# Performance work log

Hardware: AMD Instinct MI355X
Metric: run time of the kernel (lower is better)

Reference implementation:

```python
import jax, jax.numpy as jnp
import numpy as np

N, E, IN, H, OUT = 100000, 600000, 128, 128, 64
BN_EPS = 1e-5


def setup_inputs() -> dict:
    key = jax.random.key(0)
    ks = jax.random.split(key, 8)
    def lin(k, i, o):
        return jax.random.normal(k, (i, o), jnp.float32) / np.float32(np.sqrt(i))
    return {
        "x": jax.random.normal(ks[0], (N, IN), jnp.float32),
        "edge_index": jax.random.randint(ks[1], (2, E), 0, N, dtype=jnp.int64),
        "W1": lin(ks[2], IN, H), "b1": jnp.zeros((H,), jnp.float32),
        "gamma": jnp.ones((H,), jnp.float32), "beta": jnp.zeros((H,), jnp.float32),
        "W2": lin(ks[3], H, H), "b2": jnp.zeros((H,), jnp.float32),
        "Wm1": lin(ks[4], H, H), "bm1": jnp.zeros((H,), jnp.float32),
        "Wm2": lin(ks[5], H, OUT), "bm2": jnp.zeros((OUT,), jnp.float32),
    }


def reference(x, edge_index, W1, b1, gamma, beta, W2, b2, Wm1, bm1, Wm2, bm2):
    # GINConv: h = MLP((1 + eps) * x + sum_{j in N(i)} x_j), eps = 0 (train_eps=False)
    src = edge_index[0]
    dst = edge_index[1]  # PyG aggregates messages at edge_index[1]
    agg = jax.ops.segment_sum(x[src], dst, num_segments=x.shape[0])  # [N, IN]
    h = agg + x
    # inner MLP: Linear -> BatchNorm (batch stats) -> ReLU -> Linear
    h = h @ W1 + b1
    mean = jnp.mean(h, axis=0)
    var = jnp.var(h, axis=0)
    h = (h - mean) * jax.lax.rsqrt(var + BN_EPS) * gamma + beta
    h = jax.nn.relu(h)
    h = h @ W2 + b2
    h = jax.nn.relu(h)  # .relu() after conv
    # output MLP (norm=None, dropout=0.5 -> identity at inference): Linear -> ReLU -> Linear
    h = jax.nn.relu(h @ Wm1 + bm1)
    return h @ Wm2 + bm2
```

## Files before the change

kernel.cpp:

```cpp
#include <hip/hip_runtime.h>
#include <hip/hip_bf16.h>
#include <stdint.h>

#define NNODES 100000
#define NEDGES 600000
#define SCAN_CHUNK 1024
#define SCAN_NB 98

typedef __attribute__((ext_vector_type(8))) short bf16x8;
typedef __attribute__((ext_vector_type(4))) float f32x4;
typedef __attribute__((ext_vector_type(4))) unsigned int u32x4;

__device__ inline float b2f(short b) {
    union { unsigned u; float f; } v;
    v.u = ((unsigned)(unsigned short)b) << 16;
    return v.f;
}
__device__ inline short f2b(float f) {
    union { float f; unsigned u; } v;
    v.f = f;
    unsigned r = (v.u + 0x7FFFu + ((v.u >> 16) & 1u)) >> 16;
    return (short)r;
}
__device__ inline unsigned packbf(float lo, float hi) {
    return ((unsigned)(unsigned short)f2b(hi) << 16) | (unsigned)(unsigned short)f2b(lo);
}
__device__ inline void accw(float& a, float& b, unsigned w) {
    union { unsigned u; float f; } x, y;
    x.u = w << 16;
    y.u = w & 0xFFFF0000u;
    a += x.f;
    b += y.f;
}
__device__ inline int swz(int row, int kbyte) {
    return (row * 256 + kbyte) ^ ((row & 7) << 4);
}
#define MFMA16(a, b, c) __builtin_amdgcn_mfma_f32_16x16x32_bf16(a, b, c, 0, 0, 0)

__device__ inline void stage_lds(const short* __restrict__ g, short* s, int w, int l, int n) {
#pragma unroll
    for (int i = 0; i < n; ++i) {
        int base = i * 4096 + w * 1024;
        __builtin_amdgcn_global_load_lds(
            (const __attribute__((address_space(1))) void*)((const char*)g + base + l * 16),
            (__attribute__((address_space(3))) void*)((char*)s + base), 16, 0, 0);
    }
}

__global__ __launch_bounds__(256) void k_prep(const float* __restrict__ x,
                                              const float* __restrict__ W1,
                                              const float* __restrict__ W2,
                                              const float* __restrict__ Wm1,
                                              const float* __restrict__ Wm2,
                                              short* __restrict__ xb, short* __restrict__ Wt,
                                              int* __restrict__ pos, float* __restrict__ stats) {
    int i = blockIdx.x * 256 + threadIdx.x;
    if (i < (NNODES + 1) * 16) {
        bf16x8 o = (bf16x8){0, 0, 0, 0, 0, 0, 0, 0};
        if (i < NNODES * 16) {
            const float4* p = (const float4*)(x + (size_t)i * 8);
            float4 a = p[0], b = p[1];
            o[0] = f2b(a.x); o[1] = f2b(a.y); o[2] = f2b(a.z); o[3] = f2b(a.w);
            o[4] = f2b(b.x); o[5] = f2b(b.y); o[6] = f2b(b.z); o[7] = f2b(b.w);
        }
        *(bf16x8*)(xb + (size_t)i * 8) = o;
    }
    if (i < NNODES) pos[i] = 0;
    if (i < 57344) {
        int jj, lane, kt, ct;
        const float* W;
        int ldw, off;
        if (i < 16384) { off = i; W = W1; ldw = 128; }
        else if (i < 32768) { off = i - 16384; W = W2; ldw = 128; }
        else if (i < 49152) { off = i - 32768; W = Wm1; ldw = 128; }
        else { off = i - 49152; W = Wm2; ldw = 64; }
        jj = off & 7;
        lane = (off >> 3) & 63;
        kt = (off >> 9) & 3;
        ct = (off >> 11) & 7;
        int lr = lane & 15, hi = lane >> 4;
        int c = ct * 16 + lr;
        int k = kt * 32 + hi * 8 + jj;
        Wt[i] = f2b(W[k * ldw + c]);
    }
    if (i < 256) stats[i] = 0.0f;
}


__global__ __launch_bounds__(256) void k_hist(const int* __restrict__ ei, int* __restrict__ cnt) {
    int e = blockIdx.x * 256 + threadIdx.x;
    if (e < NEDGES) atomicAdd(&cnt[ei[NEDGES + e]], 1);
}

__global__ __launch_bounds__(256) void k_scan1(const int* __restrict__ cnt, int* __restrict__ bsums) {
    __shared__ int sd[256];
    int b = blockIdx.x, t = threadIdx.x;
    int base = b * SCAN_CHUNK + t * 4;
    int s = 0;
#pragma unroll
    for (int i = 0; i < 4; ++i) {
        int idx = base + i;
        if (idx < NNODES) s += cnt[idx];
    }
    sd[t] = s;
    __syncthreads();
    for (int off = 128; off > 0; off >>= 1) {
        if (t < off) sd[t] += sd[t + off];
        __syncthreads();
    }
    if (t == 0) bsums[b] = sd[0];
}

__global__ __launch_bounds__(64) void k_scan2(int* __restrict__ bsums, int* __restrict__ rowptr) {
    if (threadIdx.x == 0 && blockIdx.x == 0) {
        int run = 0;
        for (int b = 0; b < SCAN_NB; ++b) {
            int v = bsums[b];
            bsums[b] = run;
            run += v;
        }
        rowptr[NNODES] = run;
    }
}

__global__ __launch_bounds__(256) void k_scan3(const int* __restrict__ cnt,
                                               const int* __restrict__ bsums,
                                               int* __restrict__ rowptr, int* __restrict__ pos) {
    __shared__ int sd[256];
    int b = blockIdx.x, t = threadIdx.x;
    int base = b * SCAN_CHUNK + t * 4;
    int v[4];
    int s = 0;
#pragma unroll
    for (int i = 0; i < 4; ++i) {
        int idx = base + i;
        v[i] = (idx < NNODES) ? cnt[idx] : 0;
        s += v[i];
    }
    sd[t] = s;
    __syncthreads();
    for (int off = 1; off < 256; off <<= 1) {
        int val = (t >= off) ? sd[t - off] : 0;
        __syncthreads();
        sd[t] += val;
        __syncthreads();
    }
    int run = sd[t] - s + bsums[b];
#pragma unroll
    for (int i = 0; i < 4; ++i) {
        int idx = base + i;
        if (idx < NNODES) {
            rowptr[idx] = run;
            pos[idx] = run;
            run += v[i];
        }
    }
}

__global__ __launch_bounds__(256) void k_fill(const int* __restrict__ ei, int* __restrict__ pos,
                                              int* __restrict__ elist) {
    int e = blockIdx.x * 256 + threadIdx.x;
    if (e >= NEDGES) return;
    int src = ei[e];
    int dst = ei[NEDGES + e];
    int p = atomicAdd(&pos[dst], 1);
    elist[p] = src;
}

__global__ __launch_bounds__(512, 8) void k_aggstats(const short* __restrict__ xb,
                                                     const int* __restrict__ rowptr,
                                                     const int* __restrict__ elist,
                                                     const short* __restrict__ W1pk,
                                                     short* __restrict__ bufb,
                                                     float* __restrict__ stats) {
    __shared__ __align__(16) short tile[64 * 128];
    __shared__ float Sred[2][2][128];

    int t = threadIdx.x, w = t >> 6, lane = t & 63;
    int sub = lane & 31, half = lane >> 5;
    int node0 = blockIdx.x * 64;
    int nb = node0 + w * 8;
    const uint2* xr = (const uint2*)xb;

    int vr = rowptr[min(nb + min(lane, 8), NNODES)];
    int beg_all = __shfl(vr, 0);
    int tot_e = __shfl(vr, 8) - beg_all;

    int o_i[8], t_i[8];
#pragma unroll
    for (int i = 0; i < 8; ++i) {
        int beg = __shfl(vr, i);
        int end = __shfl(vr, i + 1);
        o_i[i] = beg - beg_all;
        t_i[i] = end - beg + 1;
    }

    if (tot_e <= 128) {
        int ej0 = (lane < tot_e) ? elist[beg_all + lane] : NNODES;
        int ej1 = (64 + lane < tot_e) ? elist[beg_all + 64 + lane] : NNODES;
#pragma unroll
        for (int i = 0; i < 8; ++i) {
            int n = nb + i;
            int total = t_i[i];
            float a0 = 0.f, a1 = 0.f, a2 = 0.f, a3 = 0.f;
            for (int base = 0; base < total; base += 8) {
                uint2 v[4];
#pragma unroll
                for (int k = 0; k < 4; ++k) {
                    int j = base + 2 * k + half;
                    int p = o_i[i] + j - 1;
                    int s0 = __shfl(ej0, p & 63);
                    int s1 = __shfl(ej1, p & 63);
                    int src = (p < 64) ? s0 : s1;
                    src = (j == 0) ? n : src;
                    src = (j < total && n < NNODES) ? src : NNODES;
                    v[k] = xr[(size_t)src * 32 + sub];
                }
#pragma unroll
                for (int k = 0; k < 4; ++k) {
                    accw(a0, a1, v[k].x);
                    accw(a2, a3, v[k].y);
                }
            }
            a0 += __shfl_xor(a0, 32);
            a1 += __shfl_xor(a1, 32);
            a2 += __shfl_xor(a2, 32);
            a3 += __shfl_xor(a3, 32);
            if (half == 0) {
                int row = w * 8 + i;
                int b8 = sub * 8;
                int off = swz(row, b8 & ~15) + (b8 & 8);
                uint2 o;
                o.x = packbf(a0, a1);
                o.y = packbf(a2, a3);
                *(uint2*)((char*)tile + off) = o;
            }
        }
    } else {
#pragma unroll
        for (int i = 0; i < 8; ++i) {
            int n = nb + i;
            int total = t_i[i];
            int beg = beg_all + o_i[i];
            float a0 = 0.f, a1 = 0.f, a2 = 0.f, a3 = 0.f;
            if (n < NNODES) {
                for (int base = 0; base < total; base += 64) {
                    int j = base + lane;
                    int ej = NNODES;
                    if (j < total) ej = (j == 0) ? n : elist[beg + j - 1];
                    int cnt = min(64, total - base);
                    int pairs = (cnt + 1) >> 1;
                    for (int ii = 0; ii < pairs; ii += 4) {
                        int j0 = 2 * ii + half;
                        int r0 = __shfl(ej, j0);
                        int r1 = __shfl(ej, j0 + 2);
                        int r2 = __shfl(ej, j0 + 4);
                        int r3 = __shfl(ej, j0 + 6);
                        uint2 v0 = xr[(size_t)r0 * 32 + sub];
                        uint2 v1 = xr[(size_t)r1 * 32 + sub];
                        uint2 v2 = xr[(size_t)r2 * 32 + sub];
                        uint2 v3 = xr[(size_t)r3 * 32 + sub];
                        accw(a0, a1, v0.x); accw(a2, a3, v0.y);
                        accw(a0, a1, v1.x); accw(a2, a3, v1.y);
                        accw(a0, a1, v2.x); accw(a2, a3, v2.y);
                        accw(a0, a1, v3.x); accw(a2, a3, v3.y);
                    }
                }
            }
            a0 += __shfl_xor(a0, 32);
            a1 += __shfl_xor(a1, 32);
            a2 += __shfl_xor(a2, 32);
            a3 += __shfl_xor(a3, 32);
            if (half == 0) {
                int row = w * 8 + i;
                int b8 = sub * 8;
                int off = swz(row, b8 & ~15) + (b8 & 8);
                uint2 o;
                o.x = packbf(a0, a1);
                o.y = packbf(a2, a3);
                *(uint2*)((char*)tile + off) = o;
            }
        }
    }
    __syncthreads();

    {
        int row = t >> 3, chunk = t & 7;
        int gr = node0 + row;
        if (gr < NNODES) {
            bf16x8 c0 = *(const bf16x8*)((char*)tile + swz(row, chunk * 32));
            bf16x8 c1 = *(const bf16x8*)((char*)tile + swz(row, chunk * 32 + 16));
            *(bf16x8*)(bufb + (size_t)gr * 128 + chunk * 16) = c0;
            *(bf16x8*)(bufb + (size_t)gr * 128 + chunk * 16 + 8) = c1;
        }
    }

    {
        int lr = lane & 15, hi = lane >> 4;
        int rg = w & 1, cg = w >> 1;
        f32x4 acc[2][2];
#pragma unroll
        for (int r = 0; r < 2; ++r)
#pragma unroll
            for (int c = 0; c < 2; ++c) acc[r][c] = (f32x4){0.f, 0.f, 0.f, 0.f};
#pragma unroll
        for (int kb = 0; kb < 4; ++kb) {
            int kbyte = kb * 64 + hi * 16;
            bf16x8 af[2], bw[2];
#pragma unroll
            for (int r = 0; r < 2; ++r)
                af[r] = *(const bf16x8*)((char*)tile + swz(rg * 32 + r * 16 + lr, kbyte));
#pragma unroll
            for (int c = 0; c < 2; ++c)
                bw[c] = *(const bf16x8*)(W1pk + (((cg * 2 + c) * 4 + kb) * 64 + lane) * 8);
#pragma unroll
            for (int r = 0; r < 2; ++r)
#pragma unroll
                for (int c = 0; c < 2; ++c) acc[r][c] = MFMA16(af[r], bw[c], acc[r][c]);
        }
        float s[2], q[2];
#pragma unroll
        for (int c = 0; c < 2; ++c) { s[c] = 0.f; q[c] = 0.f; }
#pragma unroll
        for (int c = 0; c < 2; ++c)
#pragma unroll
            for (int r = 0; r < 2; ++r)
#pragma unroll
                for (int rr = 0; rr < 4; ++rr) {
                    float v = acc[r][c][rr];
                    s[c] += v;
                    q[c] += v * v;
                }
#pragma unroll
        for (int c = 0; c < 2; ++c) {
            s[c] += __shfl_xor(s[c], 16); s[c] += __shfl_xor(s[c], 32);
            q[c] += __shfl_xor(q[c], 16); q[c] += __shfl_xor(q[c], 32);
        }
        if (lane < 16) {
#pragma unroll
            for (int c = 0; c < 2; ++c) {
                int col = (cg * 2 + c) * 16 + lane;
                Sred[0][rg][col] = s[c];
                Sred[1][rg][col] = q[c];
            }
        }
    }
    __syncthreads();
    if (t < 128) {
        atomicAdd(stats + t, Sred[0][0][t] + Sred[0][1][t]);
        atomicAdd(stats + 128 + t, Sred[1][0][t] + Sred[1][1][t]);
    }
}

__global__ __launch_bounds__(256, 4) void k_mlp(const short* __restrict__ bufb,
                                                const float* __restrict__ stats,
                                                const float* __restrict__ gamma,
                                                const float* __restrict__ beta,
                                                const short* __restrict__ Wt,
                                                const float* __restrict__ b2,
                                                const float* __restrict__ bm1,
                                                const float* __restrict__ bm2,
                                                float* __restrict__ out) {
    __shared__ __align__(16) short wbuf[16384];
    __shared__ float scl[3][128], shf[3][128], bm2s[64];

    int t = threadIdx.x, w = t >> 6, l = t & 63;
    int lr = l & 15, hi = l >> 4;
    size_t node0 = (size_t)blockIdx.x * 128 + w * 32;

    stage_lds(Wt, wbuf, w, l, 8);
    if (t < 128) {
        float mean = stats[t] * (1.0f / NNODES);
        float var = fmaxf(stats[128 + t] * (1.0f / NNODES) - mean * mean, 0.0f);
        float inv = rsqrtf(var + 1e-5f);
        float sc = gamma[t] * inv;
        scl[0][t] = sc;
        shf[0][t] = beta[t] - mean * sc;
        scl[1][t] = 1.0f;
        shf[1][t] = b2[t];
        scl[2][t] = 1.0f;
        shf[2][t] = bm1[t];
    }
    if (t < 64) bm2s[t] = bm2[t];

    bf16x8 bvA[4], bvB[4];
#pragma unroll
    for (int kt = 0; kt < 4; ++kt) {
        bvA[kt] = *(const bf16x8*)(bufb + (node0 + lr) * 128 + kt * 32 + hi * 8);
        bvB[kt] = *(const bf16x8*)(bufb + (node0 + 16 + lr) * 128 + kt * 32 + hi * 8);
    }
    __syncthreads();

    unsigned pwA[8][2], pwB[8][2];

    for (int g = 0; g < 3; ++g) {
#pragma unroll
        for (int ch = 0; ch < 2; ++ch) {
            f32x4 aA[4], aB[4];
#pragma unroll
            for (int cc = 0; cc < 4; ++cc) {
                aA[cc] = (f32x4){0.f, 0.f, 0.f, 0.f};
                aB[cc] = (f32x4){0.f, 0.f, 0.f, 0.f};
            }
#pragma unroll
            for (int kt = 0; kt < 4; ++kt) {
                bf16x8 wv[4];
#pragma unroll
                for (int cc = 0; cc < 4; ++cc)
                    wv[cc] = *(const bf16x8*)(wbuf + ((((ch * 4 + cc) * 4) + kt) * 64 + l) * 8);
#pragma unroll
                for (int cc = 0; cc < 4; ++cc) {
                    aA[cc] = MFMA16(wv[cc], bvA[kt], aA[cc]);
                    aB[cc] = MFMA16(wv[cc], bvB[kt], aB[cc]);
                }
            }
#pragma unroll
            for (int cc = 0; cc < 4; ++cc) {
                int ct = ch * 4 + cc;
                int c0 = ct * 16 + hi * 4;
                float4 s4 = *(const float4*)&scl[g][c0];
                float4 h4 = *(const float4*)&shf[g][c0];
                pwA[ct][0] = packbf(fmaxf(aA[cc][0] * s4.x + h4.x, 0.f),
                                    fmaxf(aA[cc][1] * s4.y + h4.y, 0.f));
                pwA[ct][1] = packbf(fmaxf(aA[cc][2] * s4.z + h4.z, 0.f),
                                    fmaxf(aA[cc][3] * s4.w + h4.w, 0.f));
                pwB[ct][0] = packbf(fmaxf(aB[cc][0] * s4.x + h4.x, 0.f),
                                    fmaxf(aB[cc][1] * s4.y + h4.y, 0.f));
                pwB[ct][1] = packbf(fmaxf(aB[cc][2] * s4.z + h4.z, 0.f),
                                    fmaxf(aB[cc][3] * s4.w + h4.w, 0.f));
            }
        }
        __syncthreads();
        if (g < 2) stage_lds(Wt + (g + 1) * 16384, wbuf, w, l, 8);
        else       stage_lds(Wt + 49152, wbuf, w, l, 4);

        {
            int h2 = hi >> 1, h1 = hi & 1;
#pragma unroll
            for (int kt = 0; kt < 4; ++kt) {
                unsigned nwA[4], nwB[4];
#pragma unroll
                for (int jp = 0; jp < 4; ++jp) {
                    int srcl = (2 * h1 + (jp >> 1)) * 16 + lr;
                    unsigned veA = (unsigned)__shfl((int)pwA[2 * kt][jp & 1], srcl);
                    unsigned voA = (unsigned)__shfl((int)pwA[2 * kt + 1][jp & 1], srcl);
                    unsigned veB = (unsigned)__shfl((int)pwB[2 * kt][jp & 1], srcl);
                    unsigned voB = (unsigned)__shfl((int)pwB[2 * kt + 1][jp & 1], srcl);
                    nwA[jp] = h2 ? voA : veA;
                    nwB[jp] = h2 ? voB : veB;
                }
                u32x4 uqA = (u32x4){nwA[0], nwA[1], nwA[2], nwA[3]};
                u32x4 uqB = (u32x4){nwB[0], nwB[1], nwB[2], nwB[3]};
                bvA[kt] = __builtin_bit_cast(bf16x8, uqA);
                bvB[kt] = __builtin_bit_cast(bf16x8, uqB);
            }
        }
        __syncthreads();
    }

#pragma unroll
    for (int ct = 0; ct < 4; ++ct) {
        f32x4 aA = (f32x4){0.f, 0.f, 0.f, 0.f};
        f32x4 aB = (f32x4){0.f, 0.f, 0.f, 0.f};
#pragma unroll
        for (int kt = 0; kt < 4; ++kt) {
            bf16x8 wv = *(const bf16x8*)(wbuf + ((ct * 4 + kt) * 64 + l) * 8);
            aA = MFMA16(bvA[kt], wv, aA);
            aB = MFMA16(bvB[kt], wv, aB);
        }
        float bias = bm2s[ct * 16 + lr];
#pragma unroll
        for (int rr = 0; rr < 4; ++rr) {
            size_t growA = node0 + hi * 4 + rr;
            size_t growB = node0 + 16 + hi * 4 + rr;
            if (growA < NNODES) out[growA * 64 + ct * 16 + lr] = aA[rr] + bias;
            if (growB < NNODES) out[growB * 64 + ct * 16 + lr] = aB[rr] + bias;
        }
    }
}

extern "C" void kernel_launch(void* const* d_in, const int* in_sizes, int n_in,
                              void* d_out, int out_size, void* d_ws, size_t ws_size,
                              hipStream_t stream) {
    const float* x     = (const float*)d_in[0];
    const int*   ei    = (const int*)d_in[1];
    const float* W1    = (const float*)d_in[2];
    const float* gamma = (const float*)d_in[4];
    const float* beta  = (const float*)d_in[5];
    const float* W2    = (const float*)d_in[6];
    const float* b2    = (const float*)d_in[7];
    const float* Wm1   = (const float*)d_in[8];
    const float* bm1   = (const float*)d_in[9];
    const float* Wm2   = (const float*)d_in[10];
    const float* bm2   = (const float*)d_in[11];
    float* out = (float*)d_out;

    char* ws = (char*)d_ws;
    short* xb    = (short*)ws;
    short* bufb  = xb + (size_t)(NNODES + 1) * 128;
    short* Wt    = bufb + (size_t)(NNODES + 128) * 128;
    float* stats = (float*)(Wt + 57344);
    int* rowptr  = (int*)(stats + 256);
    int* pos     = rowptr + (NNODES + 1);
    int* elist   = pos + NNODES;
    int* bsums   = elist + NEDGES;

    int gE = (NEDGES + 255) / 256;
    int gPrep = ((NNODES + 1) * 16 + 255) / 256;

    k_prep<<<gPrep, 256, 0, stream>>>(x, W1, W2, Wm1, Wm2, xb, Wt, pos, stats);
    k_hist<<<gE, 256, 0, stream>>>(ei, pos);
    k_scan1<<<SCAN_NB, 256, 0, stream>>>(pos, bsums);
    k_scan2<<<1, 64, 0, stream>>>(bsums, rowptr);
    k_scan3<<<SCAN_NB, 256, 0, stream>>>(pos, bsums, rowptr, pos);
    k_fill<<<gE, 256, 0, stream>>>(ei, pos, elist);

    int gAgg = (NNODES + 63) / 64;
    k_aggstats<<<gAgg, 512, 0, stream>>>(xb, rowptr, elist, Wt, bufb, stats);

    int nblkM = (NNODES + 127) / 128;
    k_mlp<<<nblkM, 256, 0, stream>>>(bufb, stats, gamma, beta, Wt, b2, bm1, bm2, out);
}
```

Baseline: 166.6 us.

## Store W1-projected activations from aggregation kernel, skipping first GEMM in MLP kernel

The aggregation kernel now writes the bf16 result of the W1 matmul (pre-BatchNorm) to global memory instead of the aggregated features, reusing the GEMM it already ran for the batch statistics. The MLP kernel then applies BN scale/shift and ReLU directly to the loaded values and starts its layer loop at the second weight matrix. This removes one redundant 128x128 GEMM per node and its weight staging. In exchange, the pre-BN activations are rounded to bf16 before normalisation, and the aggregation kernel gains an extra barrier and LDS write pass.

```diff
diff --git a/kernel.cpp b/kernel.cpp
--- a/kernel.cpp
+++ b/kernel.cpp
@@ -284,6 +284,75 @@
     }
     __syncthreads();
 
+    int lr = lane & 15, hi = lane >> 4;
+    int rg = w & 1, cg = w >> 1;
+    f32x4 uacc[2][2];
+#pragma unroll
+    for (int r = 0; r < 2; ++r)
+#pragma unroll
+        for (int c = 0; c < 2; ++c) uacc[r][c] = (f32x4){0.f, 0.f, 0.f, 0.f};
+#pragma unroll
+    for (int kb = 0; kb < 4; ++kb) {
+        int kbyte = kb * 64 + hi * 16;
+        bf16x8 af[2], bw[2];
+#pragma unroll
+        for (int r = 0; r < 2; ++r)
+            af[r] = *(const bf16x8*)((char*)tile + swz(rg * 32 + r * 16 + lr, kbyte));
+#pragma unroll
+        for (int c = 0; c < 2; ++c)
+            bw[c] = *(const bf16x8*)(W1pk + (((cg * 2 + c) * 4 + kb) * 64 + lane) * 8);
+#pragma unroll
+        for (int r = 0; r < 2; ++r)
+#pragma unroll
+            for (int c = 0; c < 2; ++c) uacc[r][c] = MFMA16(af[r], bw[c], uacc[r][c]);
+    }
+    {
+        float s[2], q[2];
+#pragma unroll
+        for (int c = 0; c < 2; ++c) { s[c] = 0.f; q[c] = 0.f; }
+#pragma unroll
+        for (int c = 0; c < 2; ++c)
+#pragma unroll
+            for (int r = 0; r < 2; ++r)
+#pragma unroll
+                for (int rr = 0; rr < 4; ++rr) {
+                    float v = uacc[r][c][rr];
+                    s[c] += v;
+                    q[c] += v * v;
+                }
+#pragma unroll
+        for (int c = 0; c < 2; ++c) {
+            s[c] += __shfl_xor(s[c], 16); s[c] += __shfl_xor(s[c], 32);
+            q[c] += __shfl_xor(q[c], 16); q[c] += __shfl_xor(q[c], 32);
+        }
+        if (lane < 16) {
+#pragma unroll
+            for (int c = 0; c < 2; ++c) {
+                int col = (cg * 2 + c) * 16 + lane;
+                Sred[0][rg][col] = s[c];
+                Sred[1][rg][col] = q[c];
+            }
+        }
+    }
+    __syncthreads();
+
+#pragma unroll
+    for (int r = 0; r < 2; ++r)
+#pragma unroll
+        for (int c = 0; c < 2; ++c)
+#pragma unroll
+            for (int rr = 0; rr < 4; ++rr) {
+                int row = rg * 32 + r * 16 + hi * 4 + rr;
+                int ch = (cg * 2 + c) * 16 + lr;
+                int off = (row * 256 + ch * 2) ^ ((row & 7) << 4);
+                *(short*)((char*)tile + off) = f2b(uacc[r][c][rr]);
+            }
+    if (t < 128) {
+        atomicAdd(stats + t, Sred[0][0][t] + Sred[0][1][t]);
+        atomicAdd(stats + 128 + t, Sred[1][0][t] + Sred[1][1][t]);
+    }
+    __syncthreads();
+
     {
         int row = t >> 3, chunk = t & 7;
         int gr = node0 + row;
@@ -293,62 +362,6 @@
             *(bf16x8*)(bufb + (size_t)gr * 128 + chunk * 16) = c0;
             *(bf16x8*)(bufb + (size_t)gr * 128 + chunk * 16 + 8) = c1;
         }
-    }
-
-    {
-        int lr = lane & 15, hi = lane >> 4;
-        int rg = w & 1, cg = w >> 1;
-        f32x4 acc[2][2];
-#pragma unroll
-        for (int r = 0; r < 2; ++r)
-#pragma unroll
-            for (int c = 0; c < 2; ++c) acc[r][c] = (f32x4){0.f, 0.f, 0.f, 0.f};
-#pragma unroll
-        for (int kb = 0; kb < 4; ++kb) {
-            int kbyte = kb * 64 + hi * 16;
-            bf16x8 af[2], bw[2];
-#pragma unroll
-            for (int r = 0; r < 2; ++r)
-                af[r] = *(const bf16x8*)((char*)tile + swz(rg * 32 + r * 16 + lr, kbyte));
-#pragma unroll
-            for (int c = 0; c < 2; ++c)
-                bw[c] = *(const bf16x8*)(W1pk + (((cg * 2 + c) * 4 + kb) * 64 + lane) * 8);
-#pragma unroll
-            for (int r = 0; r < 2; ++r)
-#pragma unroll
-                for (int c = 0; c < 2; ++c) acc[r][c] = MFMA16(af[r], bw[c], acc[r][c]);
-        }
-        float s[2], q[2];
-#pragma unroll
-        for (int c = 0; c < 2; ++c) { s[c] = 0.f; q[c] = 0.f; }
-#pragma unroll
-        for (int c = 0; c < 2; ++c)
-#pragma unroll
-            for (int r = 0; r < 2; ++r)
-#pragma unroll
-                for (int rr = 0; rr < 4; ++rr) {
-                    float v = acc[r][c][rr];
-                    s[c] += v;
-                    q[c] += v * v;
-                }
-#pragma unroll
-        for (int c = 0; c < 2; ++c) {
-            s[c] += __shfl_xor(s[c], 16); s[c] += __shfl_xor(s[c], 32);
-            q[c] += __shfl_xor(q[c], 16); q[c] += __shfl_xor(q[c], 32);
-        }
-        if (lane < 16) {
-#pragma unroll
-            for (int c = 0; c < 2; ++c) {
-                int col = (cg * 2 + c) * 16 + lane;
-                Sred[0][rg][col] = s[c];
-                Sred[1][rg][col] = q[c];
-            }
-        }
-    }
-    __syncthreads();
-    if (t < 128) {
-        atomicAdd(stats + t, Sred[0][0][t] + Sred[0][1][t]);
-        atomicAdd(stats + 128 + t, Sred[1][0][t] + Sred[1][1][t]);
     }
 }
 
@@ -368,7 +381,7 @@
     int lr = l & 15, hi = l >> 4;
     size_t node0 = (size_t)blockIdx.x * 128 + w * 32;
 
-    stage_lds(Wt, wbuf, w, l, 8);
+    stage_lds(Wt + 16384, wbuf, w, l, 8);
     if (t < 128) {
         float mean = stats[t] * (1.0f / NNODES);
         float var = fmaxf(stats[128 + t] * (1.0f / NNODES) - mean * mean, 0.0f);
@@ -391,9 +404,24 @@
     }
     __syncthreads();
 
+#pragma unroll
+    for (int kt = 0; kt < 4; ++kt) {
+        bf16x8 ia = bvA[kt], ib = bvB[kt];
+        bf16x8 oa, ob;
+#pragma unroll
+        for (int j = 0; j < 8; ++j) {
+            int ch = kt * 32 + hi * 8 + j;
+            float sc_ = scl[0][ch], sh_ = shf[0][ch];
+            oa[j] = f2b(fmaxf(b2f(ia[j]) * sc_ + sh_, 0.f));
+            ob[j] = f2b(fmaxf(b2f(ib[j]) * sc_ + sh_, 0.f));
+        }
+        bvA[kt] = oa;
+        bvB[kt] = ob;
+    }
+
     unsigned pwA[8][2], pwB[8][2];
 
-    for (int g = 0; g < 3; ++g) {
+    for (int g = 1; g < 3; ++g) {
 #pragma unroll
         for (int ch = 0; ch < 2; ++ch) {
             f32x4 aA[4], aB[4];
```

Result: no change. 164.3 us (-1.4%).
